# Optimization experiments

Measured on AMD Instinct MI355X. Metric: run time of the kernel, lower is better.

## Reference

```python
import jax, jax.numpy as jnp
import numpy as np

N = 100000   # nodes
G = 128      # graphs for mean pool


def gcn_conv(x, edge_index, W, b, num_nodes):
    # PyG GCNConv (default): x' = D^-1/2 (A+I) D^-1/2 (x W) + b
    x = x @ W
    src, dst = edge_index[0], edge_index[1]
    loop = jnp.arange(num_nodes)
    src = jnp.concatenate([src, loop])
    dst = jnp.concatenate([dst, loop])
    ones = jnp.ones(src.shape[0], x.dtype)
    deg = jax.ops.segment_sum(ones, dst, num_segments=num_nodes)
    dinv = jnp.where(deg > 0, jax.lax.rsqrt(deg), 0.0)
    norm = dinv[src] * dinv[dst]            # [E+N]
    msg = x[src] * norm[:, None]            # gather + scale
    out = jax.ops.segment_sum(msg, dst, num_segments=num_nodes)  # scatter-add
    return out + b


def setup_inputs() -> dict:
    key = jax.random.key(0)
    ks = jax.random.split(key, 5)
    x = jax.random.normal(ks[0], (N, 128), jnp.float32)
    edge_index = jax.random.randint(ks[1], (2, 1600000), 0, N)
    batch = jnp.sort(jax.random.randint(ks[2], (N,), 0, G))
    W1 = jax.random.normal(ks[3], (128, 64), jnp.float32) / np.sqrt(128.0)
    b1 = jnp.zeros((64,), jnp.float32)
    W2 = jax.random.normal(ks[4], (64, 64), jnp.float32) / np.sqrt(64.0)
    b2 = jnp.zeros((64,), jnp.float32)
    return {"x": x, "edge_index": edge_index, "batch": batch,
            "W1": W1, "b1": b1, "W2": W2, "b2": b2}


def reference(x, edge_index, batch, W1, b1, W2, b2):
    h = gcn_conv(x, edge_index, W1, b1, N)
    h = jax.nn.relu(h)  # dropout is identity in eval mode
    h = gcn_conv(h, edge_index, W2, b2, N)
    # global_mean_pool over graph ids
    s = jax.ops.segment_sum(h, batch, num_segments=G)
    cnt = jax.ops.segment_sum(jnp.ones((N,), h.dtype), batch, num_segments=G)
    return s / jnp.maximum(cnt, 1.0)[:, None]   # [G, hidden2]
```

## Files before the change

### kernel.cpp

```cpp
#include <hip/hip_runtime.h>
#include <hip/hip_fp16.h>

#define SLOTS 64

typedef _Float16 half8 __attribute__((ext_vector_type(8)));
typedef float f32x4 __attribute__((ext_vector_type(4)));

__global__ __launch_bounds__(256) void fill_pad(const int* __restrict__ src,
                                                const int* __restrict__ dst, int E, int N,
                                                int* __restrict__ deg,
                                                int* __restrict__ colpad, int chunks) {
  int range = blockIdx.x & 7;
  int chunk = blockIdx.x >> 3;
  int per = (N + 7) >> 3;
  int lo = range * per, hi = min(N, lo + per);
  int e0 = (int)((long long)chunk * E / chunks);
  int e1 = (int)((long long)(chunk + 1) * E / chunks);
  for (int e = e0 + (int)threadIdx.x; e < e1; e += 256) {
    int d = dst[e];
    if (d >= lo && d < hi) {
      int p = atomicAdd(&deg[d], 1);
      if (p < SLOTS) colpad[(size_t)p * N + d] = src[e];
    }
  }
}

__global__ __launch_bounds__(256) void calc_dinv(const int* __restrict__ deg,
                                                 float* __restrict__ dinv, int N) {
  int i = blockIdx.x * 256 + threadIdx.x;
  if (i < N) dinv[i] = rsqrtf((float)(deg[i] + 1));
}

template <int K, typename Tin>
__global__ __launch_bounds__(256) void gemm_mfma(const Tin* __restrict__ in,
                                                 const float* __restrict__ W,
                                                 const float* __restrict__ dinv,
                                                 __half* __restrict__ out,
                                                 int N, int tiles) {
  constexpr int LDK = K + 8;
  __shared__ __align__(16) _Float16 As[64][LDK];
  __shared__ __align__(16) _Float16 Wt[64][LDK];
  int t = threadIdx.x;
  for (int j = t; j < K * 64; j += 256) {
    int k = j >> 6, c = j & 63;
    Wt[c][k] = (_Float16)W[j];
  }
  int wave = t >> 6, lane = t & 63;
  int arow = lane & 15;
  int kgrp = lane >> 4;
  constexpr int C8 = K / 8;

  for (int tile = blockIdx.x; tile < tiles; tile += gridDim.x) {
    int row0 = tile * 64;
    for (int j = t; j < 64 * C8; j += 256) {
      int r = j / C8, k8 = (j % C8) * 8;
      int rr = row0 + r;
      if constexpr (sizeof(Tin) == 4) {
        half8 h = (half8)((_Float16)0.f);
        if (rr < N) {
          float4 v0 = *(const float4*)&in[(size_t)rr * K + k8];
          float4 v1 = *(const float4*)&in[(size_t)rr * K + k8 + 4];
          h[0] = (_Float16)v0.x; h[1] = (_Float16)v0.y;
          h[2] = (_Float16)v0.z; h[3] = (_Float16)v0.w;
          h[4] = (_Float16)v1.x; h[5] = (_Float16)v1.y;
          h[6] = (_Float16)v1.z; h[7] = (_Float16)v1.w;
        }
        *(half8*)&As[r][k8] = h;
      } else {
        float4 v = make_float4(0.f, 0.f, 0.f, 0.f);
        if (rr < N) v = *(const float4*)&in[(size_t)rr * K + k8];
        *(float4*)&As[r][k8] = v;
      }
    }
    __syncthreads();
    f32x4 acc[4];
#pragma unroll
    for (int ct = 0; ct < 4; ++ct) acc[ct] = (f32x4)(0.f);
#pragma unroll
    for (int kk = 0; kk < K; kk += 32) {
      half8 a = *(const half8*)&As[wave * 16 + arow][kk + kgrp * 8];
#pragma unroll
      for (int ct = 0; ct < 4; ++ct) {
        half8 b = *(const half8*)&Wt[ct * 16 + arow][kk + kgrp * 8];
        acc[ct] = __builtin_amdgcn_mfma_f32_16x16x32_f16(a, b, acc[ct], 0, 0, 0);
      }
    }
#pragma unroll
    for (int ct = 0; ct < 4; ++ct) {
#pragma unroll
      for (int r = 0; r < 4; ++r) {
        int row = row0 + wave * 16 + kgrp * 4 + r;
        if (row < N) {
          int col = ct * 16 + arow;
          out[(size_t)row * 64 + col] = __float2half(acc[ct][r] * dinv[row]);
        }
      }
    }
    __syncthreads();
  }
}

__global__ __launch_bounds__(256) void aggregate(const __half* __restrict__ g,
                                                 const int* __restrict__ deg_arr,
                                                 const int* __restrict__ colpad,
                                                 const float* __restrict__ dinv,
                                                 const float* __restrict__ bias,
                                                 const int* __restrict__ batch,
                                                 __half* __restrict__ out,
                                                 float* __restrict__ poolsum,
                                                 float* __restrict__ poolcnt,
                                                 int N, int mode) {
  int lane = threadIdx.x & 63;
  int wave = blockIdx.x * 4 + (threadIdx.x >> 6);
  int nwaves = gridDim.x * 4;
  int per = (N + nwaves - 1) / nwaves;
  int n0 = wave * per, n1 = min(N, n0 + per);
  if (n0 >= n1) return;
  float b = bias[lane];
  int cur = mode ? batch[n0] : 0;
  float pacc = 0.f, pcnt = 0.f;
  const int* myplane = colpad + (size_t)lane * N;
  for (int node = n0; node < n1; ++node) {
    int deg = min(deg_arr[node], SLOTS);
    int nb = (lane < deg) ? myplane[node] : 0;
    float a0 = __half2float(g[(size_t)node * 64 + lane]);
    float a1 = 0.f, a2 = 0.f, a3 = 0.f;
    float a4 = 0.f, a5 = 0.f, a6 = 0.f, a7 = 0.f;
    int j = 0;
    for (; j + 7 < deg; j += 8) {
      int s0 = __shfl(nb, j, 64);
      int s1 = __shfl(nb, j + 1, 64);
      int s2 = __shfl(nb, j + 2, 64);
      int s3 = __shfl(nb, j + 3, 64);
      int s4 = __shfl(nb, j + 4, 64);
      int s5 = __shfl(nb, j + 5, 64);
      int s6 = __shfl(nb, j + 6, 64);
      int s7 = __shfl(nb, j + 7, 64);
      a0 += __half2float(g[(size_t)s0 * 64 + lane]);
      a1 += __half2float(g[(size_t)s1 * 64 + lane]);
      a2 += __half2float(g[(size_t)s2 * 64 + lane]);
      a3 += __half2float(g[(size_t)s3 * 64 + lane]);
      a4 += __half2float(g[(size_t)s4 * 64 + lane]);
      a5 += __half2float(g[(size_t)s5 * 64 + lane]);
      a6 += __half2float(g[(size_t)s6 * 64 + lane]);
      a7 += __half2float(g[(size_t)s7 * 64 + lane]);
    }
    for (; j + 3 < deg; j += 4) {
      int s0 = __shfl(nb, j, 64);
      int s1 = __shfl(nb, j + 1, 64);
      int s2 = __shfl(nb, j + 2, 64);
      int s3 = __shfl(nb, j + 3, 64);
      a0 += __half2float(g[(size_t)s0 * 64 + lane]);
      a1 += __half2float(g[(size_t)s1 * 64 + lane]);
      a2 += __half2float(g[(size_t)s2 * 64 + lane]);
      a3 += __half2float(g[(size_t)s3 * 64 + lane]);
    }
    for (; j < deg; ++j) a0 += __half2float(g[(size_t)__shfl(nb, j, 64) * 64 + lane]);
    float r = dinv[node] * (((a0 + a1) + (a2 + a3)) + ((a4 + a5) + (a6 + a7))) + b;
    if (mode == 0) {
      out[(size_t)node * 64 + lane] = __float2half(fmaxf(r, 0.f));
    } else {
      int bg = batch[node];
      if (bg != cur) {
        atomicAdd(&poolsum[cur * 64 + lane], pacc);
        if (lane == 0) atomicAdd(&poolcnt[cur], pcnt);
        pacc = 0.f; pcnt = 0.f; cur = bg;
      }
      pacc += r; pcnt += 1.f;
    }
  }
  if (mode) {
    atomicAdd(&poolsum[cur * 64 + lane], pacc);
    if (lane == 0) atomicAdd(&poolcnt[cur], pcnt);
  }
}

__global__ __launch_bounds__(256) void finalize(const float* __restrict__ poolsum,
                                                const float* __restrict__ poolcnt,
                                                float* __restrict__ out, int Gn) {
  int i = blockIdx.x * 256 + threadIdx.x;
  if (i < Gn * 64) {
    float c = poolcnt[i >> 6];
    out[i] = poolsum[i] / fmaxf(c, 1.f);
  }
}

extern "C" void kernel_launch(void* const* d_in, const int* in_sizes, int n_in,
                              void* d_out, int out_size, void* d_ws, size_t ws_size,
                              hipStream_t stream) {
  const float* x   = (const float*)d_in[0];
  const int* ei    = (const int*)d_in[1];
  const int* batch = (const int*)d_in[2];
  const float* W1  = (const float*)d_in[3];
  const float* b1  = (const float*)d_in[4];
  const float* W2  = (const float*)d_in[5];
  const float* b2  = (const float*)d_in[6];
  float* out = (float*)d_out;

  int N  = in_sizes[2];
  int E  = in_sizes[1] / 2;
  int Gn = out_size / 64;

  char* ws = (char*)d_ws;
  size_t off = 0;
  auto alloc = [&](size_t bytes) -> void* {
    void* p = ws + off;
    off = (off + bytes + 255) & ~(size_t)255;
    return p;
  };
  int* deg       = (int*)alloc(4ull * N);
  float* poolsum = (float*)alloc(4ull * Gn * 64);
  float* poolcnt = (float*)alloc(4ull * Gn);
  size_t zero_bytes = off;
  int* colpad    = (int*)alloc(4ull * (size_t)N * SLOTS);
  float* dinv    = (float*)alloc(4ull * N);
  __half* gbuf   = (__half*)alloc(2ull * (size_t)N * 64);
  __half* ybuf   = (__half*)alloc(2ull * (size_t)N * 64);
  (void)ws_size; (void)n_in;

  hipMemsetAsync(d_ws, 0, zero_bytes, stream);

  const int* srcv = ei;
  const int* dstv = ei + E;
  int tiles64 = (N + 63) / 64;

  fill_pad<<<8 * 256, 256, 0, stream>>>(srcv, dstv, E, N, deg, colpad, 256);
  calc_dinv<<<(N + 255) / 256, 256, 0, stream>>>(deg, dinv, N);

  gemm_mfma<128, float><<<tiles64, 256, 0, stream>>>(x, W1, dinv, gbuf, N, tiles64);
  aggregate<<<2048, 256, 0, stream>>>(gbuf, deg, colpad, dinv, b1, batch, ybuf,
                                      nullptr, nullptr, N, 0);
  gemm_mfma<64, __half><<<tiles64, 256, 0, stream>>>(ybuf, W2, dinv, gbuf, N, tiles64);
  aggregate<<<2048, 256, 0, stream>>>(gbuf, deg, colpad, dinv, b2, batch, nullptr,
                                      poolsum, poolcnt, N, 1);
  finalize<<<(Gn * 64 + 255) / 256, 256, 0, stream>>>(poolsum, poolcnt, out, Gn);
}
```

Baseline: 311.9 us.

## Switch adjacency to node-major layout, pad degree counters, register-load GEMM A

```diff
diff --git a/kernel.cpp b/kernel.cpp
--- a/kernel.cpp
+++ b/kernel.cpp
@@ -2,13 +2,14 @@
 #include <hip/hip_fp16.h>
 
 #define SLOTS 64
+#define DEGSTRIDE 16
 
 typedef _Float16 half8 __attribute__((ext_vector_type(8)));
 typedef float f32x4 __attribute__((ext_vector_type(4)));
 
 __global__ __launch_bounds__(256) void fill_pad(const int* __restrict__ src,
                                                 const int* __restrict__ dst, int E, int N,
-                                                int* __restrict__ deg,
+                                                int* __restrict__ degp,
                                                 int* __restrict__ colpad, int chunks) {
   int range = blockIdx.x & 7;
   int chunk = blockIdx.x >> 3;
@@ -19,16 +20,21 @@
   for (int e = e0 + (int)threadIdx.x; e < e1; e += 256) {
     int d = dst[e];
     if (d >= lo && d < hi) {
-      int p = atomicAdd(&deg[d], 1);
-      if (p < SLOTS) colpad[(size_t)p * N + d] = src[e];
-    }
-  }
-}
-
-__global__ __launch_bounds__(256) void calc_dinv(const int* __restrict__ deg,
-                                                 float* __restrict__ dinv, int N) {
+      int p = atomicAdd(&degp[(size_t)d * DEGSTRIDE], 1);
+      if (p < SLOTS) colpad[(size_t)d * SLOTS + p] = src[e];
+    }
+  }
+}
+
+__global__ __launch_bounds__(256) void calc_dinv(const int* __restrict__ degp,
+                                                 float* __restrict__ dinv,
+                                                 int* __restrict__ degc, int N) {
   int i = blockIdx.x * 256 + threadIdx.x;
-  if (i < N) dinv[i] = rsqrtf((float)(deg[i] + 1));
+  if (i < N) {
+    int d = degp[(size_t)i * DEGSTRIDE];
+    dinv[i] = rsqrtf((float)(d + 1));
+    degc[i] = min(d, SLOTS);
+  }
 }
 
 template <int K, typename Tin>
@@ -38,70 +44,68 @@
                                                  __half* __restrict__ out,
                                                  int N, int tiles) {
   constexpr int LDK = K + 8;
-  __shared__ __align__(16) _Float16 As[64][LDK];
   __shared__ __align__(16) _Float16 Wt[64][LDK];
   int t = threadIdx.x;
   for (int j = t; j < K * 64; j += 256) {
     int k = j >> 6, c = j & 63;
     Wt[c][k] = (_Float16)W[j];
   }
+  __syncthreads();
   int wave = t >> 6, lane = t & 63;
-  int arow = lane & 15;
-  int kgrp = lane >> 4;
-  constexpr int C8 = K / 8;
+  int arow = lane & 15, kgrp = lane >> 4;
+  constexpr int KK = K / 32;
 
   for (int tile = blockIdx.x; tile < tiles; tile += gridDim.x) {
     int row0 = tile * 64;
-    for (int j = t; j < 64 * C8; j += 256) {
-      int r = j / C8, k8 = (j % C8) * 8;
-      int rr = row0 + r;
-      if constexpr (sizeof(Tin) == 4) {
-        half8 h = (half8)((_Float16)0.f);
-        if (rr < N) {
-          float4 v0 = *(const float4*)&in[(size_t)rr * K + k8];
-          float4 v1 = *(const float4*)&in[(size_t)rr * K + k8 + 4];
+    int row = row0 + wave * 16 + arow;
+    half8 af[KK];
+    if (row < N) {
+#pragma unroll
+      for (int kk = 0; kk < KK; ++kk) {
+        if constexpr (sizeof(Tin) == 4) {
+          const float4* p = (const float4*)&in[(size_t)row * K + kk * 32 + kgrp * 8];
+          float4 v0 = p[0], v1 = p[1];
+          half8 h;
           h[0] = (_Float16)v0.x; h[1] = (_Float16)v0.y;
           h[2] = (_Float16)v0.z; h[3] = (_Float16)v0.w;
           h[4] = (_Float16)v1.x; h[5] = (_Float16)v1.y;
           h[6] = (_Float16)v1.z; h[7] = (_Float16)v1.w;
+          af[kk] = h;
+        } else {
+          af[kk] = *(const half8*)&in[(size_t)row * K + kk * 32 + kgrp * 8];
         }
-        *(half8*)&As[r][k8] = h;
-      } else {
-        float4 v = make_float4(0.f, 0.f, 0.f, 0.f);
-        if (rr < N) v = *(const float4*)&in[(size_t)rr * K + k8];
-        *(float4*)&As[r][k8] = v;
-      }
-    }
-    __syncthreads();
+      }
+    } else {
+#pragma unroll
+      for (int kk = 0; kk < KK; ++kk) af[kk] = (half8)((_Float16)0.f);
+    }
     f32x4 acc[4];
 #pragma unroll
     for (int ct = 0; ct < 4; ++ct) acc[ct] = (f32x4)(0.f);
 #pragma unroll
-    for (int kk = 0; kk < K; kk += 32) {
-      half8 a = *(const half8*)&As[wave * 16 + arow][kk + kgrp * 8];
+    for (int kk = 0; kk < KK; ++kk) {
 #pragma unroll
       for (int ct = 0; ct < 4; ++ct) {
-        half8 b = *(const half8*)&Wt[ct * 16 + arow][kk + kgrp * 8];
-        acc[ct] = __builtin_amdgcn_mfma_f32_16x16x32_f16(a, b, acc[ct], 0, 0, 0);
-      }
-    }
-#pragma unroll
-    for (int ct = 0; ct < 4; ++ct) {
-#pragma unroll
-      for (int r = 0; r < 4; ++r) {
-        int row = row0 + wave * 16 + kgrp * 4 + r;
-        if (row < N) {
-          int col = ct * 16 + arow;
-          out[(size_t)row * 64 + col] = __float2half(acc[ct][r] * dinv[row]);
-        }
-      }
-    }
-    __syncthreads();
+        half8 b = *(const half8*)&Wt[ct * 16 + arow][kk * 32 + kgrp * 8];
+        acc[ct] = __builtin_amdgcn_mfma_f32_16x16x32_f16(af[kk], b, acc[ct], 0, 0, 0);
+      }
+    }
+    int rbase = row0 + wave * 16 + kgrp * 4;
+#pragma unroll
+    for (int r = 0; r < 4; ++r) {
+      int rr = rbase + r;
+      if (rr < N) {
+        float s = dinv[rr];
+#pragma unroll
+        for (int ct = 0; ct < 4; ++ct)
+          out[(size_t)rr * 64 + ct * 16 + arow] = __float2half(acc[ct][r] * s);
+      }
+    }
   }
 }
 
 __global__ __launch_bounds__(256) void aggregate(const __half* __restrict__ g,
-                                                 const int* __restrict__ deg_arr,
+                                                 const int* __restrict__ degc,
                                                  const int* __restrict__ colpad,
                                                  const float* __restrict__ dinv,
                                                  const float* __restrict__ bias,
@@ -119,10 +123,12 @@
   float b = bias[lane];
   int cur = mode ? batch[n0] : 0;
   float pacc = 0.f, pcnt = 0.f;
-  const int* myplane = colpad + (size_t)lane * N;
+  int deg = degc[n0];
+  int nb = colpad[(size_t)n0 * SLOTS + lane];
   for (int node = n0; node < n1; ++node) {
-    int deg = min(deg_arr[node], SLOTS);
-    int nb = (lane < deg) ? myplane[node] : 0;
+    int nxt = (node + 1 < n1) ? node + 1 : node;
+    int dn = degc[nxt];
+    int nbn = colpad[(size_t)nxt * SLOTS + lane];
     float a0 = __half2float(g[(size_t)node * 64 + lane]);
     float a1 = 0.f, a2 = 0.f, a3 = 0.f;
     float a4 = 0.f, a5 = 0.f, a6 = 0.f, a7 = 0.f;
@@ -157,6 +163,8 @@
     }
     for (; j < deg; ++j) a0 += __half2float(g[(size_t)__shfl(nb, j, 64) * 64 + lane]);
     float r = dinv[node] * (((a0 + a1) + (a2 + a3)) + ((a4 + a5) + (a6 + a7))) + b;
+    deg = dn;
+    nb = nbn;
     if (mode == 0) {
       out[(size_t)node * 64 + lane] = __float2half(fmaxf(r, 0.f));
     } else {
@@ -208,30 +216,32 @@
     off = (off + bytes + 255) & ~(size_t)255;
     return p;
   };
-  int* deg       = (int*)alloc(4ull * N);
   float* poolsum = (float*)alloc(4ull * Gn * 64);
   float* poolcnt = (float*)alloc(4ull * Gn);
   size_t zero_bytes = off;
   int* colpad    = (int*)alloc(4ull * (size_t)N * SLOTS);
   float* dinv    = (float*)alloc(4ull * N);
+  int* degc      = (int*)alloc(4ull * N);
   __half* gbuf   = (__half*)alloc(2ull * (size_t)N * 64);
   __half* ybuf   = (__half*)alloc(2ull * (size_t)N * 64);
+  int* degp = (int*)gbuf;
   (void)ws_size; (void)n_in;
 
-  hipMemsetAsync(d_ws, 0, zero_bytes, stream);
+  hipMemsetAsync(poolsum, 0, zero_bytes, stream);
+  hipMemsetAsync(degp, 0, 4ull * (size_t)N * DEGSTRIDE, stream);
 
   const int* srcv = ei;
   const int* dstv = ei + E;
   int tiles64 = (N + 63) / 64;
 
-  fill_pad<<<8 * 256, 256, 0, stream>>>(srcv, dstv, E, N, deg, colpad, 256);
-  calc_dinv<<<(N + 255) / 256, 256, 0, stream>>>(deg, dinv, N);
+  fill_pad<<<8 * 256, 256, 0, stream>>>(srcv, dstv, E, N, degp, colpad, 256);
+  calc_dinv<<<(N + 255) / 256, 256, 0, stream>>>(degp, dinv, degc, N);
 
   gemm_mfma<128, float><<<tiles64, 256, 0, stream>>>(x, W1, dinv, gbuf, N, tiles64);
-  aggregate<<<2048, 256, 0, stream>>>(gbuf, deg, colpad, dinv, b1, batch, ybuf,
+  aggregate<<<2048, 256, 0, stream>>>(gbuf, degc, colpad, dinv, b1, batch, ybuf,
                                       nullptr, nullptr, N, 0);
   gemm_mfma<64, __half><<<tiles64, 256, 0, stream>>>(ybuf, W2, dinv, gbuf, N, tiles64);
-  aggregate<<<2048, 256, 0, stream>>>(gbuf, deg, colpad, dinv, b2, batch, nullptr,
+  aggregate<<<2048, 256, 0, stream>>>(gbuf, degc, colpad, dinv, b2, batch, nullptr,
                                       poolsum, poolcnt, N, 1);
   finalize<<<(Gn * 64 + 255) / 256, 256, 0, stream>>>(poolsum, poolcnt, out, Gn);
 }
```

New measurement: 309.8 us. Within noise of the previous version (-0.7%).
